# Optimization experiments

Hardware: AMD Instinct MI355X
Metric: run time of the kernel (lower is better)

The kernel has to match this reference:

```python
import jax, jax.numpy as jnp
import numpy as np

WINDOW_SIZES = (4, 8, 16)
STRIDE_FACTOR = 0.5
EPS = 1e-6


def _pool_scale(x, mask_f, w, stride):
    # x: [B,T,D], mask_f: [B,T] float. Overlapping masked mean via prefix sums.
    B, T, D = x.shape
    xm = x * mask_f[:, :, None]
    cx = jnp.concatenate([jnp.zeros((B, 1, D), x.dtype), jnp.cumsum(xm, axis=1)], axis=1)  # [B,T+1,D]
    cm = jnp.concatenate([jnp.zeros((B, 1), x.dtype), jnp.cumsum(mask_f, axis=1)], axis=1)  # [B,T+1]
    starts = jnp.arange(0, T - w + 1, stride)  # [S]
    num = cx[:, starts + w, :] - cx[:, starts, :]          # [B,S,D] masked window sums
    valid = cm[:, starts + w] - cm[:, starts]              # [B,S] valid counts
    avg = num / jnp.clip(valid, EPS)[:, :, None]
    return avg, valid > 0


def setup_inputs() -> dict:
    key = jax.random.key(0)
    k1, k2 = jax.random.split(key)
    B, T, D = 8, 4096, 512
    x = jax.random.normal(k1, (B, T, D), dtype=jnp.float32)
    mask = jax.random.bernoulli(k2, 0.9, (B, T))  # bool, True=valid
    return {"x": x, "mask": mask}


def reference(x, mask):
    mask_f = mask.astype(x.dtype)
    vis_list, msk_list = [], []
    for w in WINDOW_SIZES:
        stride = max(1, int(w * STRIDE_FACTOR))
        avg, m = _pool_scale(x, mask_f, w, stride)
        vis_list.append(avg)
        msk_list.append(m)
    return (*vis_list, *msk_list)
```

## Files before the change

kernel.cpp:

```cpp
#include <hip/hip_runtime.h>


#define EPS 1e-6f

constexpr int B = 8, T = 4096, D = 512;
constexpr int TILE = 64;
constexpr int HALO = 8;
constexpr int NT = TILE + HALO;
constexpr int NP = NT / 2;
constexpr int S4 = 2047, S8 = 1023, S16 = 511;

constexpr size_t OFF0 = 0;
constexpr size_t OFF1 = (size_t)B * S4 * D;
constexpr size_t OFF2 = OFF1 + (size_t)B * S8 * D;
constexpr size_t OFF3 = OFF2 + (size_t)B * S16 * D;
constexpr size_t OFF4 = OFF3 + (size_t)B * S4;
constexpr size_t OFF5 = OFF4 + (size_t)B * S8;

__global__ __launch_bounds__(256)
void tpp_kernel(const float* __restrict__ x,
                const int* __restrict__ mask,
                float* __restrict__ out) {
  const int tid  = threadIdx.x;
  const int b    = blockIdx.z;
  const int tile = blockIdx.y;
  const int d    = blockIdx.x * 256 + tid;
  const int t0   = tile * TILE;

  __shared__ float sm[NT];
  __shared__ float sc2[NP];
  __shared__ float inv4[TILE / 2];
  __shared__ float inv8[TILE / 4];
  __shared__ float inv16[TILE / 8];

  if (tid < NT) {
    int t = t0 + tid;
    sm[tid] = (t < T && mask[b * T + t] != 0) ? 1.0f : 0.0f;
  }
  __syncthreads();
  if (tid < NP) sc2[tid] = sm[2 * tid] + sm[2 * tid + 1];
  __syncthreads();

  if (tid < 32) {
    float c = sc2[tid] + sc2[tid + 1];
    inv4[tid] = 1.0f / fmaxf(c, EPS);
    if (blockIdx.x == 0) {
      int s = tile * 32 + tid;
      if (s < S4) out[OFF3 + (size_t)b * S4 + s] = (c > 0.f) ? 1.f : 0.f;
    }
  } else if (tid < 48) {
    int k = tid - 32;
    float c = sc2[2 * k] + sc2[2 * k + 1] + sc2[2 * k + 2] + sc2[2 * k + 3];
    inv8[k] = 1.0f / fmaxf(c, EPS);
    if (blockIdx.x == 0) {
      int s = tile * 16 + k;
      if (s < S8) out[OFF4 + (size_t)b * S8 + s] = (c > 0.f) ? 1.f : 0.f;
    }
  } else if (tid < 56) {
    int l = tid - 48;
    float c = 0.f;
#pragma unroll
    for (int i = 0; i < 8; ++i) c += sc2[4 * l + i];
    inv16[l] = 1.0f / fmaxf(c, EPS);
    if (blockIdx.x == 0) {
      int s = tile * 8 + l;
      if (s < S16) out[OFF5 + (size_t)b * S16 + s] = (c > 0.f) ? 1.f : 0.f;
    }
  }
  __syncthreads();

  const float* xb = x + (size_t)b * T * D + d;
  float p[NP];
#pragma unroll
  for (int i = 0; i < NP; ++i) {
    int t = t0 + 2 * i;
    float a0 = 0.f, a1 = 0.f;
    if (t < T) {
      a0 = xb[(size_t)t * D];
      a1 = xb[(size_t)(t + 1) * D];
    }
    p[i] = a0 * sm[2 * i] + a1 * sm[2 * i + 1];
  }

  float* o4 = out + OFF0 + ((size_t)b * S4 + (size_t)tile * 32) * D + d;
#pragma unroll
  for (int j = 0; j < 32; ++j) {
    int s = tile * 32 + j;
    if (s < S4) o4[(size_t)j * D] = (p[j] + p[j + 1]) * inv4[j];
  }

  float* o8 = out + OFF1 + ((size_t)b * S8 + (size_t)tile * 16) * D + d;
#pragma unroll
  for (int k = 0; k < 16; ++k) {
    int s = tile * 16 + k;
    if (s < S8)
      o8[(size_t)k * D] =
          (p[2 * k] + p[2 * k + 1] + p[2 * k + 2] + p[2 * k + 3]) * inv8[k];
  }

  float* o16 = out + OFF2 + ((size_t)b * S16 + (size_t)tile * 8) * D + d;
#pragma unroll
  for (int l = 0; l < 8; ++l) {
    int s = tile * 8 + l;
    if (s < S16) {
      float sum = 0.f;
#pragma unroll
      for (int i = 0; i < 8; ++i) sum += p[4 * l + i];
      o16[(size_t)l * D] = sum * inv16[l];
    }
  }
}

extern "C" void kernel_launch(void* const* d_in, const int* in_sizes, int n_in,
                              void* d_out, int out_size, void* d_ws, size_t ws_size,
                              hipStream_t stream) {
  const float* x   = (const float*)d_in[0];
  const int* mask  = (const int*)d_in[1];
  float* out       = (float*)d_out;
  dim3 grid(D / 256, T / TILE, B);
  tpp_kernel<<<grid, 256, 0, stream>>>(x, mask, out);
}
```

Before: 113.2 us.

## Vectorize to float4 per thread, halve time tile, add nontemporal stores and guard specialization

Each thread now handles four consecutive D elements through float4 loads and stores, and one 128-thread block covers the full D width. The time tile shrinks from 64 to 32 steps, so the grid grows along T. Output writes use nontemporal stores, and a templated path drops bounds checks for every tile except the last. The aim is wider memory transactions and less cache pollution from the large streaming output. The trade-off is a larger halo re-read fraction (8 of 40 rows instead of 8 of 72) and more register pressure from f4 arrays.

```diff
diff --git a/kernel.cpp b/kernel.cpp
--- a/kernel.cpp
+++ b/kernel.cpp
@@ -3,11 +3,14 @@
 
 #define EPS 1e-6f
 
-constexpr int B = 8, T = 4096, D = 512;
-constexpr int TILE = 64;
+typedef float f4 __attribute__((ext_vector_type(4)));
+
+constexpr int B = 8, T = 4096, D = 512, D4 = D / 4;
+constexpr int TILE = 32;
 constexpr int HALO = 8;
 constexpr int NT = TILE + HALO;
 constexpr int NP = NT / 2;
+constexpr int NTILES = T / TILE;
 constexpr int S4 = 2047, S8 = 1023, S16 = 511;
 
 constexpr size_t OFF0 = 0;
@@ -17,21 +20,68 @@
 constexpr size_t OFF4 = OFF3 + (size_t)B * S4;
 constexpr size_t OFF5 = OFF4 + (size_t)B * S8;
 
-__global__ __launch_bounds__(256)
-void tpp_kernel(const float* __restrict__ x,
-                const int* __restrict__ mask,
+template <bool GUARD>
+__device__ __forceinline__ void compute_store(
+    const f4* __restrict__ xb,
+    const float* sm, const float* inv4s, const float* inv8s,
+    const float* inv16s, float* __restrict__ out, int b, int tile, int tid) {
+  const int t0 = tile * TILE;
+
+  f4 p[NP];
+#pragma unroll
+  for (int i = 0; i < NP; ++i) {
+    int t = t0 + 2 * i;
+    f4 a0 = {0.f, 0.f, 0.f, 0.f}, a1 = {0.f, 0.f, 0.f, 0.f};
+    if (!GUARD || t < T) {
+      a0 = xb[(size_t)t * D4];
+      a1 = xb[(size_t)(t + 1) * D4];
+    }
+    p[i] = a0 * sm[2 * i] + a1 * sm[2 * i + 1];
+  }
+
+  f4* o4 = (f4*)(out + OFF0) + ((size_t)b * S4 + (size_t)tile * 16) * D4 + tid;
+#pragma unroll
+  for (int j = 0; j < 16; ++j) {
+    if (!GUARD || (tile * 16 + j) < S4) {
+      f4 v = (p[j] + p[j + 1]) * inv4s[j];
+      __builtin_nontemporal_store(v, o4 + (size_t)j * D4);
+    }
+  }
+
+  f4* o8 = (f4*)(out + OFF1) + ((size_t)b * S8 + (size_t)tile * 8) * D4 + tid;
+#pragma unroll
+  for (int k = 0; k < 8; ++k) {
+    if (!GUARD || (tile * 8 + k) < S8) {
+      f4 v = (p[2 * k] + p[2 * k + 1] + p[2 * k + 2] + p[2 * k + 3]) * inv8s[k];
+      __builtin_nontemporal_store(v, o8 + (size_t)k * D4);
+    }
+  }
+
+  f4* o16 =
+      (f4*)(out + OFF2) + ((size_t)b * S16 + (size_t)tile * 4) * D4 + tid;
+#pragma unroll
+  for (int l = 0; l < 4; ++l) {
+    if (!GUARD || (tile * 4 + l) < S16) {
+      f4 v = {0.f, 0.f, 0.f, 0.f};
+#pragma unroll
+      for (int i = 0; i < 8; ++i) v += p[4 * l + i];
+      v *= inv16s[l];
+      __builtin_nontemporal_store(v, o16 + (size_t)l * D4);
+    }
+  }
+}
+
+__global__ __launch_bounds__(128)
+void tpp_kernel(const f4* __restrict__ x4, const int* __restrict__ mask,
                 float* __restrict__ out) {
-  const int tid  = threadIdx.x;
-  const int b    = blockIdx.z;
+  const int tid = threadIdx.x;
+  const int b = blockIdx.z;
   const int tile = blockIdx.y;
-  const int d    = blockIdx.x * 256 + tid;
-  const int t0   = tile * TILE;
+  const int t0 = tile * TILE;
 
   __shared__ float sm[NT];
   __shared__ float sc2[NP];
-  __shared__ float inv4[TILE / 2];
-  __shared__ float inv8[TILE / 4];
-  __shared__ float inv16[TILE / 8];
+  __shared__ float inv4s[16], inv8s[8], inv16s[4];
 
   if (tid < NT) {
     int t = t0 + tid;
@@ -41,82 +91,41 @@
   if (tid < NP) sc2[tid] = sm[2 * tid] + sm[2 * tid + 1];
   __syncthreads();
 
-  if (tid < 32) {
+  if (tid < 16) {
     float c = sc2[tid] + sc2[tid + 1];
-    inv4[tid] = 1.0f / fmaxf(c, EPS);
-    if (blockIdx.x == 0) {
-      int s = tile * 32 + tid;
-      if (s < S4) out[OFF3 + (size_t)b * S4 + s] = (c > 0.f) ? 1.f : 0.f;
-    }
-  } else if (tid < 48) {
-    int k = tid - 32;
+    inv4s[tid] = 1.0f / fmaxf(c, EPS);
+    int s = tile * 16 + tid;
+    if (s < S4) out[OFF3 + (size_t)b * S4 + s] = (c > 0.f) ? 1.f : 0.f;
+  } else if (tid < 24) {
+    int k = tid - 16;
     float c = sc2[2 * k] + sc2[2 * k + 1] + sc2[2 * k + 2] + sc2[2 * k + 3];
-    inv8[k] = 1.0f / fmaxf(c, EPS);
-    if (blockIdx.x == 0) {
-      int s = tile * 16 + k;
-      if (s < S8) out[OFF4 + (size_t)b * S8 + s] = (c > 0.f) ? 1.f : 0.f;
-    }
-  } else if (tid < 56) {
-    int l = tid - 48;
+    inv8s[k] = 1.0f / fmaxf(c, EPS);
+    int s = tile * 8 + k;
+    if (s < S8) out[OFF4 + (size_t)b * S8 + s] = (c > 0.f) ? 1.f : 0.f;
+  } else if (tid < 28) {
+    int l = tid - 24;
     float c = 0.f;
 #pragma unroll
     for (int i = 0; i < 8; ++i) c += sc2[4 * l + i];
-    inv16[l] = 1.0f / fmaxf(c, EPS);
-    if (blockIdx.x == 0) {
-      int s = tile * 8 + l;
-      if (s < S16) out[OFF5 + (size_t)b * S16 + s] = (c > 0.f) ? 1.f : 0.f;
-    }
+    inv16s[l] = 1.0f / fmaxf(c, EPS);
+    int s = tile * 4 + l;
+    if (s < S16) out[OFF5 + (size_t)b * S16 + s] = (c > 0.f) ? 1.f : 0.f;
   }
   __syncthreads();
 
-  const float* xb = x + (size_t)b * T * D + d;
-  float p[NP];
-#pragma unroll
-  for (int i = 0; i < NP; ++i) {
-    int t = t0 + 2 * i;
-    float a0 = 0.f, a1 = 0.f;
-    if (t < T) {
-      a0 = xb[(size_t)t * D];
-      a1 = xb[(size_t)(t + 1) * D];
-    }
-    p[i] = a0 * sm[2 * i] + a1 * sm[2 * i + 1];
-  }
-
-  float* o4 = out + OFF0 + ((size_t)b * S4 + (size_t)tile * 32) * D + d;
-#pragma unroll
-  for (int j = 0; j < 32; ++j) {
-    int s = tile * 32 + j;
-    if (s < S4) o4[(size_t)j * D] = (p[j] + p[j + 1]) * inv4[j];
-  }
-
-  float* o8 = out + OFF1 + ((size_t)b * S8 + (size_t)tile * 16) * D + d;
-#pragma unroll
-  for (int k = 0; k < 16; ++k) {
-    int s = tile * 16 + k;
-    if (s < S8)
-      o8[(size_t)k * D] =
-          (p[2 * k] + p[2 * k + 1] + p[2 * k + 2] + p[2 * k + 3]) * inv8[k];
-  }
-
-  float* o16 = out + OFF2 + ((size_t)b * S16 + (size_t)tile * 8) * D + d;
-#pragma unroll
-  for (int l = 0; l < 8; ++l) {
-    int s = tile * 8 + l;
-    if (s < S16) {
-      float sum = 0.f;
-#pragma unroll
-      for (int i = 0; i < 8; ++i) sum += p[4 * l + i];
-      o16[(size_t)l * D] = sum * inv16[l];
-    }
-  }
+  const f4* xb = x4 + (size_t)b * T * D4 + tid;
+  if (tile < NTILES - 1)
+    compute_store<false>(xb, sm, inv4s, inv8s, inv16s, out, b, tile, tid);
+  else
+    compute_store<true>(xb, sm, inv4s, inv8s, inv16s, out, b, tile, tid);
 }
 
 extern "C" void kernel_launch(void* const* d_in, const int* in_sizes, int n_in,
-                              void* d_out, int out_size, void* d_ws, size_t ws_size,
-                              hipStream_t stream) {
-  const float* x   = (const float*)d_in[0];
-  const int* mask  = (const int*)d_in[1];
-  float* out       = (float*)d_out;
-  dim3 grid(D / 256, T / TILE, B);
-  tpp_kernel<<<grid, 256, 0, stream>>>(x, mask, out);
+                              void* d_out, int out_size, void* d_ws,
+                              size_t ws_size, hipStream_t stream) {
+  const f4* x4 = (const f4*)d_in[0];
+  const int* mask = (const int*)d_in[1];
+  float* out = (float*)d_out;
+  dim3 grid(1, NTILES, B);
+  tpp_kernel<<<grid, 128, 0, stream>>>(x4, mask, out);
 }
```

New measurement: 110.7 us. 1.02x faster.
